# Performance work log

Hardware: AMD Instinct MI355X
Metric: run time of the kernel (lower is better)

## Reference

```python
import jax, jax.numpy as jnp
import numpy as np

# FP4 E2M1 representable magnitudes (sign handled separately)
_FP4_GRID = np.array([0.0, 0.5, 1.0, 1.5, 2.0, 3.0, 4.0, 6.0], dtype=np.float32)
_FP4_MIDS = (_FP4_GRID[:-1] + _FP4_GRID[1:]) / 2.0  # round-to-nearest boundaries


def fp4_quant_dequant(w):
    """Per-tensor absmax-scaled round-to-nearest FP4 (E2M1) fake quantization."""
    grid = jnp.asarray(_FP4_GRID, dtype=w.dtype)
    mids = jnp.asarray(_FP4_MIDS, dtype=w.dtype)
    scale = jnp.max(jnp.abs(w)) / 6.0  # map absmax -> top FP4 level
    a = jnp.abs(w) / scale
    idx = jnp.searchsorted(mids, a)  # nearest grid index via boundary search
    return grid[idx] * jnp.sign(w) * scale


def fp4_linear(x, W, b):
    # dequantized-weight matmul + bias, as in FP4Linear
    Wq = fp4_quant_dequant(W)
    return x @ Wq.T + b


def setup_inputs() -> dict:
    key = jax.random.key(0)
    k1, k2, k3, k4, k5 = jax.random.split(key, 5)
    B, D_IN, D_H, D_OUT = 8192, 2048, 8192, 2048
    x = jax.random.normal(k1, (B, D_IN), dtype=jnp.float32)
    W1 = jax.random.normal(k2, (D_H, D_IN), dtype=jnp.float32) * 0.02
    b1 = jax.random.normal(k3, (D_H,), dtype=jnp.float32) * 0.02
    W2 = jax.random.normal(k4, (D_OUT, D_H), dtype=jnp.float32) * 0.02
    b2 = jax.random.normal(k5, (D_OUT,), dtype=jnp.float32) * 0.02
    return {"x": x, "W1": W1, "b1": b1, "W2": W2, "b2": b2}


def reference(x, W1, b1, W2, b2):
    h = jax.nn.relu(fp4_linear(x, W1, b1))  # [B, hidden]
    y = fp4_linear(h, W2, b2)                # [B, out]
    return y
```

## Files before the change

kernel.cpp:

```cpp
#include <hip/hip_runtime.h>
#include <hip/hip_bf16.h>
#include <stdint.h>

typedef __attribute__((ext_vector_type(8))) short short8;
typedef __attribute__((ext_vector_type(4))) float f32x4;

#define AS1 __attribute__((address_space(1)))
#define AS3 __attribute__((address_space(3)))

static __device__ __forceinline__ unsigned short f2bf(float f) {
    unsigned int u = __float_as_uint(f);
    u += 0x7FFFu + ((u >> 16) & 1u);
    return (unsigned short)(u >> 16);
}

__global__ void init_amax(unsigned int* amax) {
    if (threadIdx.x < 2) amax[threadIdx.x] = 0u;
}

__global__ void absmax_kernel(const float4* __restrict__ w, size_t n4,
                              unsigned int* __restrict__ out) {
    float m = 0.0f;
    size_t i = (size_t)blockIdx.x * blockDim.x + threadIdx.x;
    size_t stride = (size_t)gridDim.x * blockDim.x;
    for (; i < n4; i += stride) {
        float4 v = w[i];
        m = fmaxf(m, fmaxf(fmaxf(fabsf(v.x), fabsf(v.y)),
                           fmaxf(fabsf(v.z), fabsf(v.w))));
    }
    #pragma unroll
    for (int off = 32; off > 0; off >>= 1)
        m = fmaxf(m, __shfl_down(m, off, 64));
    __shared__ float sm[4];
    int lane = threadIdx.x & 63, wid = threadIdx.x >> 6;
    if (lane == 0) sm[wid] = m;
    __syncthreads();
    if (threadIdx.x == 0) {
        float bm = fmaxf(fmaxf(sm[0], sm[1]), fmaxf(sm[2], sm[3]));
        atomicMax(out, __float_as_uint(bm));
    }
}

static __device__ __forceinline__ unsigned short quant_one(float wv, float scale) {
    float a = fabsf(wv) / scale;
    int idx = (a > 0.25f) + (a > 0.75f) + (a > 1.25f) + (a > 1.75f)
            + (a > 2.5f)  + (a > 3.5f)  + (a > 5.0f);
    const unsigned long long lo = 0x3FC03F803F000000ull;
    const unsigned long long hi = 0x40C0408040404000ull;
    unsigned long long tab = (idx < 4) ? lo : hi;
    unsigned short mag = (unsigned short)(tab >> ((idx & 3) * 16));
    unsigned short sgn = (unsigned short)((__float_as_uint(wv) >> 16) & 0x8000u);
    return (unsigned short)(mag | sgn);
}

__global__ void quant_kernel(const float4* __restrict__ w, size_t n4,
                             const unsigned int* __restrict__ amax,
                             ushort4* __restrict__ q) {
    const float scale = __uint_as_float(*amax) / 6.0f;
    size_t i = (size_t)blockIdx.x * blockDim.x + threadIdx.x;
    size_t stride = (size_t)gridDim.x * blockDim.x;
    for (; i < n4; i += stride) {
        float4 v = w[i];
        ushort4 o;
        o.x = quant_one(v.x, scale);
        o.y = quant_one(v.y, scale);
        o.z = quant_one(v.z, scale);
        o.w = quant_one(v.w, scale);
        q[i] = o;
    }
}

__global__ void cast_bf16_kernel(const float4* __restrict__ x, size_t n4,
                                 ushort4* __restrict__ o) {
    size_t i = (size_t)blockIdx.x * blockDim.x + threadIdx.x;
    size_t stride = (size_t)gridDim.x * blockDim.x;
    for (; i < n4; i += stride) {
        float4 v = x[i];
        ushort4 r;
        r.x = f2bf(v.x); r.y = f2bf(v.y); r.z = f2bf(v.z); r.w = f2bf(v.w);
        o[i] = r;
    }
}


#define GLL(gp, dst)                                                    \
    __builtin_amdgcn_global_load_lds((const AS1 unsigned int*)(gp),     \
        (AS3 unsigned int*)(dst), 16, 0, 0)

#define STG(gp, ldsoff)                                       \
    do {                                                      \
        GLL((gp) + goff0, lds + (ldsoff) + tid * 16);         \
        GLL((gp) + goff1, lds + (ldsoff) + 8192 + tid * 16);  \
    } while (0)

#define LD4(dst, base, s0)                                                    \
    do {                                                                      \
        _Pragma("unroll") for (int _i = 0; _i < 4; ++_i)                      \
            dst[_i] = *(const short8*)((base) + ((s0) + _i * 2) * 1024);      \
    } while (0)

#define MFG(AH, ARR, BRR)                                                      \
    do {                                                                       \
        _Pragma("unroll") for (int _i = 0; _i < 4; ++_i)                       \
            _Pragma("unroll") for (int _j = 0; _j < 4; ++_j)                   \
                acc[(AH) * 4 + _i][_j] =                                       \
                    __builtin_amdgcn_mfma_f32_16x16x32_bf16(                   \
                        ARR[_i], BRR[_j], acc[(AH) * 4 + _i][_j], 0, 0, 0);    \
    } while (0)

#define BAR()  __builtin_amdgcn_s_barrier()
#define PRIO(x) __builtin_amdgcn_s_setprio(x)
#define SCHB() __builtin_amdgcn_sched_barrier(0)
#define LGKM(n) do { SCHB(); asm volatile("s_waitcnt lgkmcnt(" #n ")"); SCHB(); } while (0)

#define KTILE(ldsB_, ldsA_, MA1, kA1, oA1, MORE, kNXT, oB0, oB1, oA0, VMODE)   \
    do {                                                                       \
        LD4(bE, ldsB_, 0);                                  \
        LD4(aP, ldsA_, 0);                                     \
        LD4(aQ, ldsA_, 8);                                     \
        if (MA1) STG(pA1 + (kA1), oA1);                                        \
        LGKM(4);                                \
        PRIO(1); MFG(0, aP, bE); PRIO(0);                                      \
        LD4(bO, ldsB_, 1);                                        \
        LD4(aP, ldsA_, 1);                                     \
        LGKM(8);                               \
        PRIO(1); MFG(1, aQ, bE); PRIO(0);                                      \
        LD4(aQ, ldsA_, 9);                                     \
        LGKM(4);                              \
        PRIO(1); MFG(0, aP, bO); PRIO(0);                                      \
        LGKM(0);                            \
        BAR();                                                                 \
        if (MORE) { STG(pB0 + (kNXT), oB0); STG(pB1 + (kNXT), oB1);            \
                    STG(pA0 + (kNXT), oA0); }                                  \
        SCHB();                                                                \
        PRIO(1); MFG(1, aQ, bO); PRIO(0);                                      \
        if (VMODE == 2) { asm volatile("s_waitcnt vmcnt(6)"); }                \
        if (VMODE == 1) { asm volatile("s_waitcnt vmcnt(0)"); }                \
        BAR();                                                                 \
    } while (0)

template <int RELU_BF16>
__global__ __launch_bounds__(512, 2)
void gemm8(const unsigned short* __restrict__ A,
           const unsigned short* __restrict__ B,
           const float* __restrict__ bias,
           const unsigned int* __restrict__ amax,
           float* __restrict__ outF,
           unsigned short* __restrict__ outH,
           int M, int N, int K, int gx) {
    __shared__ __align__(16) char lds[131072];

    const int tid  = threadIdx.x;
    const int lane = tid & 63;
    const int wid  = tid >> 6;
    const int wm   = wid >> 2;
    const int wn   = wid & 3;

    const int nwg = gridDim.x;
    const int wg  = blockIdx.x;
    const int swz = (wg & 7) * (nwg >> 3) + (wg >> 3);
    const int bx  = swz % gx;
    const int by  = swz / gx;
    const int col0 = bx * 256;
    const int row0 = by * 256;

    int sp = ((lane & 15) << 6) + ((lane >> 4) << 4);
    sp ^= ((sp >> 9) & 1) << 5;

    const char* ldsA_E = lds + wm * 16384 + sp;
    const char* ldsB_E = lds + 32768 + (wn >> 1) * 16384 + (wn & 1) * 8192 + sp;
    const char* ldsA_O = ldsA_E + 65536;
    const char* ldsB_O = ldsB_E + 65536;

    int goff0, goff1;
    {
        int o = tid * 16;
        int s = o >> 10, b = o & 1023;
        b ^= ((b >> 9) & 1) << 5;
        goff0 = (((s >> 1) << 4) + (b >> 6)) * K + ((s & 1) << 5) + ((b & 63) >> 1);
        o = 8192 + tid * 16;
        s = o >> 10; b = o & 1023;
        b ^= ((b >> 9) & 1) << 5;
        goff1 = (((s >> 1) << 4) + (b >> 6)) * K + ((s & 1) << 5) + ((b & 63) >> 1);
    }
    const unsigned short* pA0 = A + (size_t)row0 * K;
    const unsigned short* pA1 = A + (size_t)(row0 + 128) * K;
    const unsigned short* pB0 = B + (size_t)col0 * K;
    const unsigned short* pB1 = B + (size_t)(col0 + 128) * K;

    STG(pB0, 32768); STG(pB1, 49152); STG(pA0, 0); STG(pA1, 16384);
    STG(pB0 + 64, 98304); STG(pB1 + 64, 114688); STG(pA0 + 64, 65536);
    asm volatile("s_waitcnt vmcnt(6)");
    BAR();

    f32x4 acc[8][4] = {};
    short8 aP[4], aQ[4], bE[4], bO[4];
    const int NIT = K >> 7;

    for (int it = 0; it < NIT - 1; ++it) {
        const int o0 = it * 128;
        KTILE(ldsB_E, ldsA_E, 1, o0 + 64, 81920,
              1, o0 + 128, 32768, 49152, 0, 2);
        KTILE(ldsB_O, ldsA_O, 1, o0 + 128, 16384,
              1, o0 + 192, 98304, 114688, 65536, 2);
    }
    {
        const int o0 = (NIT - 1) * 128;
        KTILE(ldsB_E, ldsA_E, 1, o0 + 64, 81920,
              0, 0, 0, 0, 0, 1);
        KTILE(ldsB_O, ldsA_O, 0, 0, 0,
              0, 0, 0, 0, 0, 0);
    }

    const float scale = __uint_as_float(*amax) / 6.0f;
    #pragma unroll
    for (int j = 0; j < 4; ++j) {
        const int col = col0 + wn * 64 + j * 16 + (lane & 15);
        const float bvv = bias[col];
        #pragma unroll
        for (int i = 0; i < 8; ++i) {
            const int rbase = row0 + wm * 128 + i * 16 + (lane >> 4) * 4;
            #pragma unroll
            for (int r = 0; r < 4; ++r) {
                float v = acc[i][j][r] * scale + bvv;
                if (RELU_BF16) {
                    v = fmaxf(v, 0.0f);
                    outH[(size_t)(rbase + r) * N + col] = f2bf(v);
                } else {
                    outF[(size_t)(rbase + r) * N + col] = v;
                }
            }
        }
    }
}

extern "C" void kernel_launch(void* const* d_in, const int* in_sizes, int n_in,
                              void* d_out, int out_size, void* d_ws, size_t ws_size,
                              hipStream_t stream) {
    const float* x  = (const float*)d_in[0];
    const float* W1 = (const float*)d_in[1];
    const float* b1 = (const float*)d_in[2];
    const float* W2 = (const float*)d_in[3];
    const float* b2 = (const float*)d_in[4];
    float* out = (float*)d_out;

    const int Bm = 8192, Din = 2048, Dh = 8192, Dout = 2048;
    const size_t nW1 = (size_t)Dh * Din;
    const size_t nW2 = (size_t)Dout * Dh;
    const size_t nX  = (size_t)Bm * Din;
    const size_t nH  = (size_t)Bm * Dh;

    const size_t need = 256 + 2 * (nW1 + nW2 + nX + nH);
    if (ws_size < need) return;

    uint8_t* ws = (uint8_t*)d_ws;
    unsigned int*   amax = (unsigned int*)ws;
    unsigned short* Q1 = (unsigned short*)(ws + 256);
    unsigned short* Q2 = Q1 + nW1;
    unsigned short* Xb = Q2 + nW2;
    unsigned short* H  = Xb + nX;

    init_amax<<<1, 64, 0, stream>>>(amax);
    absmax_kernel<<<1024, 256, 0, stream>>>((const float4*)W1, nW1 / 4, amax + 0);
    absmax_kernel<<<1024, 256, 0, stream>>>((const float4*)W2, nW2 / 4, amax + 1);
    quant_kernel<<<2048, 256, 0, stream>>>((const float4*)W1, nW1 / 4, amax + 0, (ushort4*)Q1);
    quant_kernel<<<2048, 256, 0, stream>>>((const float4*)W2, nW2 / 4, amax + 1, (ushort4*)Q2);
    cast_bf16_kernel<<<2048, 256, 0, stream>>>((const float4*)x, nX / 4, (ushort4*)Xb);

    gemm8<1><<<dim3((Dh / 256) * (Bm / 256)), 512, 0, stream>>>(
        Xb, Q1, b1, amax + 0, nullptr, H, Bm, Dh, Din, Dh / 256);
    gemm8<0><<<dim3((Dout / 256) * (Bm / 256)), 512, 0, stream>>>(
        H, Q2, b2, amax + 1, out, nullptr, Bm, Dout, Dh, Dout / 256);
}
```

Measured before the change: 569.1 us.

## Switch GEMM to 32x32x16 bf16 MFMA with restructured LDS fragment loads

Replaces the 16x16x32 MFMA tiling with 32x32x16 bf16 MFMAs. Each wave now holds a 4x2 grid of 32x32 accumulators, and the LDS read addressing is recomputed to build 32x32 fragments. The prefetch schedule moves both A halves together and the vmcnt waits change to match. The larger MFMA shape cuts the number of LDS fragment loads and MFMA issues per FLOP, at the cost of a new LDS access pattern that may introduce bank conflicts and a different pipelining order.

After: 1.308 ms, median of 2. +129.9%, slower.

```diff
diff --git a/kernel.cpp b/kernel.cpp
--- a/kernel.cpp
+++ b/kernel.cpp
@@ -3,7 +3,7 @@
 #include <stdint.h>
 
 typedef __attribute__((ext_vector_type(8))) short short8;
-typedef __attribute__((ext_vector_type(4))) float f32x4;
+typedef __attribute__((ext_vector_type(16))) float f32x16;
 
 #define AS1 __attribute__((address_space(1)))
 #define AS3 __attribute__((address_space(3)))
@@ -93,19 +93,30 @@
         GLL((gp) + goff1, lds + (ldsoff) + 8192 + tid * 16);  \
     } while (0)
 
-#define LD4(dst, base, s0)                                                    \
+#define LDA8(dst, base, ksbase)                                               \
     do {                                                                      \
-        _Pragma("unroll") for (int _i = 0; _i < 4; ++_i)                      \
-            dst[_i] = *(const short8*)((base) + ((s0) + _i * 2) * 1024);      \
-    } while (0)
-
-#define MFG(AH, ARR, BRR)                                                      \
+        _Pragma("unroll") for (int _m = 0; _m < 4; ++_m)                      \
+            _Pragma("unroll") for (int _k = 0; _k < 2; ++_k)                  \
+                dst[_m * 2 + _k] = *(const short8*)((base) + _m * 4096 +      \
+                                                    sp32[(ksbase) + _k]);     \
+    } while (0)
+
+#define LDB4(dst, base, ksbase)                                               \
+    do {                                                                      \
+        _Pragma("unroll") for (int _n = 0; _n < 2; ++_n)                      \
+            _Pragma("unroll") for (int _k = 0; _k < 2; ++_k)                  \
+                dst[_n * 2 + _k] = *(const short8*)((base) + _n * 4096 +      \
+                                                    sp32[(ksbase) + _k]);     \
+    } while (0)
+
+#define MFK(ARR, BRR)                                                          \
     do {                                                                       \
-        _Pragma("unroll") for (int _i = 0; _i < 4; ++_i)                       \
-            _Pragma("unroll") for (int _j = 0; _j < 4; ++_j)                   \
-                acc[(AH) * 4 + _i][_j] =                                       \
-                    __builtin_amdgcn_mfma_f32_16x16x32_bf16(                   \
-                        ARR[_i], BRR[_j], acc[(AH) * 4 + _i][_j], 0, 0, 0);    \
+        _Pragma("unroll") for (int _m = 0; _m < 4; ++_m)                       \
+            _Pragma("unroll") for (int _n = 0; _n < 2; ++_n)                   \
+                _Pragma("unroll") for (int _k = 0; _k < 2; ++_k)               \
+                    acc[_m][_n] = __builtin_amdgcn_mfma_f32_32x32x16_bf16(     \
+                        ARR[_m * 2 + _k], BRR[_n * 2 + _k], acc[_m][_n],       \
+                        0, 0, 0);                                              \
     } while (0)
 
 #define BAR()  __builtin_amdgcn_s_barrier()
@@ -113,28 +124,21 @@
 #define SCHB() __builtin_amdgcn_sched_barrier(0)
 #define LGKM(n) do { SCHB(); asm volatile("s_waitcnt lgkmcnt(" #n ")"); SCHB(); } while (0)
 
-#define KTILE(ldsB_, ldsA_, MA1, kA1, oA1, MORE, kNXT, oB0, oB1, oA0, VMODE)   \
+#define KTILE32(ldsB_, ldsA_, MA, kA, oA0_, oA1_, MB, kB, oB0_, oB1_, VMODE)   \
     do {                                                                       \
-        LD4(bE, ldsB_, 0);                                  \
-        LD4(aP, ldsA_, 0);                                     \
-        LD4(aQ, ldsA_, 8);                                     \
-        if (MA1) STG(pA1 + (kA1), oA1);                                        \
-        LGKM(4);                                \
-        PRIO(1); MFG(0, aP, bE); PRIO(0);                                      \
-        LD4(bO, ldsB_, 1);                                        \
-        LD4(aP, ldsA_, 1);                                     \
-        LGKM(8);                               \
-        PRIO(1); MFG(1, aQ, bE); PRIO(0);                                      \
-        LD4(aQ, ldsA_, 9);                                     \
-        LGKM(4);                              \
-        PRIO(1); MFG(0, aP, bO); PRIO(0);                                      \
+        LDA8(aP, ldsA_, 0);                       \
+        LDB4(b0, ldsB_, 0);                             \
+        if (MA) { STG(pA0 + (kA), oA0_); STG(pA1 + (kA), oA1_); }              \
+        LDB4(b1, ldsB_, 2);                                    \
+        LDA8(aQ, ldsA_, 2);                                    \
+        LGKM(12);                            \
+        PRIO(1); MFK(aP, b0); PRIO(0);                                         \
         LGKM(0);                            \
         BAR();                                                                 \
-        if (MORE) { STG(pB0 + (kNXT), oB0); STG(pB1 + (kNXT), oB1);            \
-                    STG(pA0 + (kNXT), oA0); }                                  \
+        if (MB) { STG(pB0 + (kB), oB0_); STG(pB1 + (kB), oB1_); }              \
         SCHB();                                                                \
-        PRIO(1); MFG(1, aQ, bO); PRIO(0);                                      \
-        if (VMODE == 2) { asm volatile("s_waitcnt vmcnt(6)"); }                \
+        PRIO(1); MFK(aQ, b1); PRIO(0);                                         \
+        if (VMODE == 2) { asm volatile("s_waitcnt vmcnt(4)"); }                \
         if (VMODE == 1) { asm volatile("s_waitcnt vmcnt(0)"); }                \
         BAR();                                                                 \
     } while (0)
@@ -164,11 +168,20 @@
     const int col0 = bx * 256;
     const int row0 = by * 256;
 
-    int sp = ((lane & 15) << 6) + ((lane >> 4) << 4);
-    sp ^= ((sp >> 9) & 1) << 5;
-
-    const char* ldsA_E = lds + wm * 16384 + sp;
-    const char* ldsB_E = lds + 32768 + (wn >> 1) * 16384 + (wn & 1) * 8192 + sp;
+    int sp32[4];
+    {
+        const int l = lane;
+        const int base16 = ((l >> 4) & 1) * 2048;
+        const int inner0 = ((l & 15) << 6) + (((l >> 5) & 1) << 4);
+        const int flip = ((l >> 3) & 1) << 5;
+        #pragma unroll
+        for (int ks = 0; ks < 4; ++ks)
+            sp32[ks] = base16 + (ks >> 1) * 1024 +
+                       ((inner0 + ((ks & 1) << 5)) ^ flip);
+    }
+
+    const char* ldsA_E = lds + wm * 16384;
+    const char* ldsB_E = lds + 32768 + wn * 8192;
     const char* ldsA_O = ldsA_E + 65536;
     const char* ldsB_O = ldsB_E + 65536;
 
@@ -189,45 +202,46 @@
     const unsigned short* pB1 = B + (size_t)(col0 + 128) * K;
 
     STG(pB0, 32768); STG(pB1, 49152); STG(pA0, 0); STG(pA1, 16384);
-    STG(pB0 + 64, 98304); STG(pB1 + 64, 114688); STG(pA0 + 64, 65536);
-    asm volatile("s_waitcnt vmcnt(6)");
+    STG(pB0 + 64, 98304); STG(pB1 + 64, 114688);
+    asm volatile("s_waitcnt vmcnt(4)");
     BAR();
 
-    f32x4 acc[8][4] = {};
-    short8 aP[4], aQ[4], bE[4], bO[4];
-    const int NIT = K >> 7;
-
-    for (int it = 0; it < NIT - 1; ++it) {
+    f32x16 acc[4][2] = {};
+    short8 aP[8], aQ[8], b0[4], b1[4];
+    const int NIT2 = K >> 7;
+
+    for (int it = 0; it < NIT2 - 1; ++it) {
         const int o0 = it * 128;
-        KTILE(ldsB_E, ldsA_E, 1, o0 + 64, 81920,
-              1, o0 + 128, 32768, 49152, 0, 2);
-        KTILE(ldsB_O, ldsA_O, 1, o0 + 128, 16384,
-              1, o0 + 192, 98304, 114688, 65536, 2);
+        KTILE32(ldsB_E, ldsA_E, 1, o0 + 64, 65536, 81920,
+                1, o0 + 128, 32768, 49152, 2);
+        KTILE32(ldsB_O, ldsA_O, 1, o0 + 128, 0, 16384,
+                1, o0 + 192, 98304, 114688, 2);
     }
     {
-        const int o0 = (NIT - 1) * 128;
-        KTILE(ldsB_E, ldsA_E, 1, o0 + 64, 81920,
-              0, 0, 0, 0, 0, 1);
-        KTILE(ldsB_O, ldsA_O, 0, 0, 0,
-              0, 0, 0, 0, 0, 0);
+        const int o0 = (NIT2 - 1) * 128;
+        KTILE32(ldsB_E, ldsA_E, 1, o0 + 64, 65536, 81920,
+                0, 0, 0, 0, 1);
+        KTILE32(ldsB_O, ldsA_O, 0, 0, 0, 0,
+                0, 0, 0, 0, 0);
     }
 
     const float scale = __uint_as_float(*amax) / 6.0f;
     #pragma unroll
-    for (int j = 0; j < 4; ++j) {
-        const int col = col0 + wn * 64 + j * 16 + (lane & 15);
+    for (int nb = 0; nb < 2; ++nb) {
+        const int col = col0 + wn * 64 + nb * 32 + (lane & 31);
         const float bvv = bias[col];
         #pragma unroll
-        for (int i = 0; i < 8; ++i) {
-            const int rbase = row0 + wm * 128 + i * 16 + (lane >> 4) * 4;
+        for (int mb = 0; mb < 4; ++mb) {
+            const int rbase = row0 + wm * 128 + mb * 32 + ((lane >> 5) & 1) * 4;
             #pragma unroll
-            for (int r = 0; r < 4; ++r) {
-                float v = acc[i][j][r] * scale + bvv;
+            for (int r = 0; r < 16; ++r) {
+                const int row = rbase + (r & 3) + 8 * (r >> 2);
+                float v = acc[mb][nb][r] * scale + bvv;
                 if (RELU_BF16) {
                     v = fmaxf(v, 0.0f);
-                    outH[(size_t)(rbase + r) * N + col] = f2bf(v);
+                    outH[(size_t)row * N + col] = f2bf(v);
                 } else {
-                    outF[(size_t)(rbase + r) * N + col] = v;
+                    outF[(size_t)row * N + col] = v;
                 }
             }
         }
```

## Store hidden activations in tiled layout, stage fp32 epilogue via LDS, regroup tiles

Applied to the files above, without the earlier changes.

The first GEMM now writes H in a 16x16-tiled layout, so the second GEMM's A-operand loads read contiguous 512-byte chunks instead of strided rows. The fp32 output epilogue of the second GEMM is staged through LDS with a swizzle, so each thread writes 16-byte vectors to global memory instead of scattered 4-byte stores. Workgroup-to-tile mapping changes to per-XCD rectangular chunks of width cw, intended to improve L2 reuse. The cost is a more complex addressing scheme and extra barriers in the epilogue.

Result: faster. 534.2 us (median of 3 runs) (-6.1%).

```diff
diff --git a/kernel.cpp b/kernel.cpp
--- a/kernel.cpp
+++ b/kernel.cpp
@@ -87,11 +87,20 @@
     __builtin_amdgcn_global_load_lds((const AS1 unsigned int*)(gp),     \
         (AS3 unsigned int*)(dst), 16, 0, 0)
 
-#define STG(gp, ldsoff)                                       \
-    do {                                                      \
-        GLL((gp) + goff0, lds + (ldsoff) + tid * 16);         \
-        GLL((gp) + goff1, lds + (ldsoff) + 8192 + tid * 16);  \
-    } while (0)
+#define STGA(gp, ldsoff)                                        \
+    do {                                                        \
+        GLL((gp) + goffA0, lds + (ldsoff) + tid * 16);          \
+        GLL((gp) + goffA1, lds + (ldsoff) + 8192 + tid * 16);   \
+    } while (0)
+
+#define STGB(gp, ldsoff)                                        \
+    do {                                                        \
+        GLL((gp) + goffB0, lds + (ldsoff) + tid * 16);          \
+        GLL((gp) + goffB1, lds + (ldsoff) + 8192 + tid * 16);   \
+    } while (0)
+
+#define KAB(e) ((size_t)(e) * (LAYA ? 32 : 2))
+#define KBB(e) ((size_t)(e) * 2)
 
 #define LD4(dst, base, s0)                                                    \
     do {                                                                      \
@@ -118,7 +127,7 @@
         LD4(bE, ldsB_, 0);                                  \
         LD4(aP, ldsA_, 0);                                     \
         LD4(aQ, ldsA_, 8);                                     \
-        if (MA1) STG(pA1 + (kA1), oA1);                                        \
+        if (MA1) STGA(pA1 + KAB(kA1), oA1);                                    \
         LGKM(4);                                \
         PRIO(1); MFG(0, aP, bE); PRIO(0);                                      \
         LD4(bO, ldsB_, 1);                                        \
@@ -130,8 +139,8 @@
         PRIO(1); MFG(0, aP, bO); PRIO(0);                                      \
         LGKM(0);                            \
         BAR();                                                                 \
-        if (MORE) { STG(pB0 + (kNXT), oB0); STG(pB1 + (kNXT), oB1);            \
-                    STG(pA0 + (kNXT), oA0); }                                  \
+        if (MORE) { STGB(pB0 + KBB(kNXT), oB0); STGB(pB1 + KBB(kNXT), oB1);    \
+                    STGA(pA0 + KAB(kNXT), oA0); }                              \
         SCHB();                                                                \
         PRIO(1); MFG(1, aQ, bO); PRIO(0);                                      \
         if (VMODE == 2) { asm volatile("s_waitcnt vmcnt(6)"); }                \
@@ -139,15 +148,15 @@
         BAR();                                                                 \
     } while (0)
 
-template <int RELU_BF16>
+template <int RELU_BF16, int LAYA>
 __global__ __launch_bounds__(512, 2)
-void gemm8(const unsigned short* __restrict__ A,
+void gemm8(const char* __restrict__ A,
            const unsigned short* __restrict__ B,
            const float* __restrict__ bias,
            const unsigned int* __restrict__ amax,
            float* __restrict__ outF,
-           unsigned short* __restrict__ outH,
-           int M, int N, int K, int gx) {
+           char* __restrict__ outH,
+           int M, int N, int K, int gx, int cw) {
     __shared__ __align__(16) char lds[131072];
 
     const int tid  = threadIdx.x;
@@ -158,9 +167,14 @@
 
     const int nwg = gridDim.x;
     const int wg  = blockIdx.x;
-    const int swz = (wg & 7) * (nwg >> 3) + (wg >> 3);
-    const int bx  = swz % gx;
-    const int by  = swz / gx;
+    const int c   = wg & 7;
+    const int idx = wg >> 3;
+    const int nc  = nwg >> 3;
+    const int cxc = gx / cw;
+    const int ox  = (c % cxc) * cw;
+    const int oy  = (c / cxc) * (nc / cw);
+    const int bx  = ox + idx % cw;
+    const int by  = oy + idx / cw;
     const int col0 = bx * 256;
     const int row0 = by * 256;
 
@@ -172,24 +186,32 @@
     const char* ldsA_O = ldsA_E + 65536;
     const char* ldsB_O = ldsB_E + 65536;
 
-    int goff0, goff1;
+    int goffA0, goffA1, goffB0, goffB1;
     {
-        int o = tid * 16;
-        int s = o >> 10, b = o & 1023;
-        b ^= ((b >> 9) & 1) << 5;
-        goff0 = (((s >> 1) << 4) + (b >> 6)) * K + ((s & 1) << 5) + ((b & 63) >> 1);
-        o = 8192 + tid * 16;
-        s = o >> 10; b = o & 1023;
-        b ^= ((b >> 9) & 1) << 5;
-        goff1 = (((s >> 1) << 4) + (b >> 6)) * K + ((s & 1) << 5) + ((b & 63) >> 1);
-    }
-    const unsigned short* pA0 = A + (size_t)row0 * K;
-    const unsigned short* pA1 = A + (size_t)(row0 + 128) * K;
-    const unsigned short* pB0 = B + (size_t)col0 * K;
-    const unsigned short* pB1 = B + (size_t)(col0 + 128) * K;
-
-    STG(pB0, 32768); STG(pB1, 49152); STG(pA0, 0); STG(pA1, 16384);
-    STG(pB0 + 64, 98304); STG(pB1 + 64, 114688); STG(pA0 + 64, 65536);
+        #pragma unroll
+        for (int h = 0; h < 2; ++h) {
+            int o = h * 8192 + tid * 16;
+            int s = o >> 10, b = o & 1023;
+            b ^= ((b >> 9) & 1) << 5;
+            int row = ((s >> 1) << 4) + (b >> 6);
+            int k   = ((s & 1) << 5) + ((b & 63) >> 1);
+            int gB  = (row * K + k) * 2;
+            int gA  = LAYA ? ((row >> 4) * 262144 + (k >> 4) * 512 +
+                              (row & 3) * 128 + ((row >> 2) & 3) * 32 + (k & 15) * 2)
+                           : gB;
+            if (h == 0) { goffA0 = gA; goffB0 = gB; }
+            else        { goffA1 = gA; goffB1 = gB; }
+        }
+    }
+    const char* pA0 = A + (LAYA ? (size_t)row0 * 16384 : (size_t)row0 * K * 2);
+    const char* pA1 = A + (LAYA ? (size_t)(row0 + 128) * 16384
+                                : (size_t)(row0 + 128) * K * 2);
+    const char* pB0 = (const char*)B + (size_t)col0 * K * 2;
+    const char* pB1 = (const char*)B + (size_t)(col0 + 128) * K * 2;
+
+    STGB(pB0, 32768); STGB(pB1, 49152); STGA(pA0, 0); STGA(pA1, 16384);
+    STGB(pB0 + KBB(64), 98304); STGB(pB1 + KBB(64), 114688);
+    STGA(pA0 + KAB(64), 65536);
     asm volatile("s_waitcnt vmcnt(6)");
     BAR();
 
@@ -213,23 +235,57 @@
     }
 
     const float scale = __uint_as_float(*amax) / 6.0f;
-    #pragma unroll
-    for (int j = 0; j < 4; ++j) {
-        const int col = col0 + wn * 64 + j * 16 + (lane & 15);
-        const float bvv = bias[col];
+
+    if (RELU_BF16) {
+        const int gbit = (lane >> 4) * 32 + (lane & 15) * 2;
         #pragma unroll
-        for (int i = 0; i < 8; ++i) {
-            const int rbase = row0 + wm * 128 + i * 16 + (lane >> 4) * 4;
+        for (int j = 0; j < 4; ++j) {
+            const int col = col0 + wn * 64 + j * 16 + (lane & 15);
+            const float bvv = bias[col];
+            const size_t ktb = (size_t)((col0 >> 4) + wn * 4 + j) * 512;
             #pragma unroll
-            for (int r = 0; r < 4; ++r) {
-                float v = acc[i][j][r] * scale + bvv;
-                if (RELU_BF16) {
-                    v = fmaxf(v, 0.0f);
-                    outH[(size_t)(rbase + r) * N + col] = f2bf(v);
-                } else {
-                    outF[(size_t)(rbase + r) * N + col] = v;
+            for (int i = 0; i < 8; ++i) {
+                const size_t rtb = (size_t)(((row0 + wm * 128) >> 4) + i) * 262144;
+                #pragma unroll
+                for (int r = 0; r < 4; ++r) {
+                    float v = fmaxf(acc[i][j][r] * scale + bvv, 0.0f);
+                    *(unsigned short*)(outH + rtb + ktb + r * 128 + gbit) = f2bf(v);
                 }
             }
+        }
+    } else {
+        #pragma unroll
+        for (int p = 0; p < 2; ++p) {
+            if (wm == p) {
+                #pragma unroll
+                for (int j = 0; j < 4; ++j) {
+                    const int colb = wn * 64 + j * 16 + (lane & 15);
+                    const float bvv = bias[col0 + colb];
+                    #pragma unroll
+                    for (int i = 0; i < 8; ++i) {
+                        #pragma unroll
+                        for (int r = 0; r < 4; ++r) {
+                            const int row_l = i * 16 + (lane >> 4) * 4 + r;
+                            const int blk = (colb >> 2) ^ (((row_l >> 2) & 3) << 2);
+                            *(float*)(lds + row_l * 1024 + blk * 16 + (colb & 3) * 4)
+                                = acc[i][j][r] * scale + bvv;
+                        }
+                    }
+                }
+            }
+            asm volatile("s_waitcnt lgkmcnt(0)");
+            BAR();
+            #pragma unroll
+            for (int q = 0; q < 16; ++q) {
+                const int flat  = q * 8192 + tid * 16;
+                const int row_l = flat >> 10;
+                const int blk0  = (flat >> 4) & 63;
+                const int blk   = blk0 ^ (((row_l >> 2) & 3) << 2);
+                f32x4 v = *(const f32x4*)(lds + row_l * 1024 + blk * 16);
+                *(f32x4*)(outF + (size_t)(row0 + p * 128 + row_l) * N
+                                 + col0 + blk0 * 4) = v;
+            }
+            BAR();
         }
     }
 }
@@ -258,7 +314,7 @@
     unsigned short* Q1 = (unsigned short*)(ws + 256);
     unsigned short* Q2 = Q1 + nW1;
     unsigned short* Xb = Q2 + nW2;
-    unsigned short* H  = Xb + nX;
+    char*           H  = (char*)(Xb + nX);
 
     init_amax<<<1, 64, 0, stream>>>(amax);
     absmax_kernel<<<1024, 256, 0, stream>>>((const float4*)W1, nW1 / 4, amax + 0);
@@ -267,8 +323,10 @@
     quant_kernel<<<2048, 256, 0, stream>>>((const float4*)W2, nW2 / 4, amax + 1, (ushort4*)Q2);
     cast_bf16_kernel<<<2048, 256, 0, stream>>>((const float4*)x, nX / 4, (ushort4*)Xb);
 
-    gemm8<1><<<dim3((Dh / 256) * (Bm / 256)), 512, 0, stream>>>(
-        Xb, Q1, b1, amax + 0, nullptr, H, Bm, Dh, Din, Dh / 256);
-    gemm8<0><<<dim3((Dout / 256) * (Bm / 256)), 512, 0, stream>>>(
-        H, Q2, b2, amax + 1, out, nullptr, Bm, Dout, Dh, Dout / 256);
-}
+    gemm8<1, 0><<<dim3((Dh / 256) * (Bm / 256)), 512, 0, stream>>>(
+        (const char*)Xb, Q1, b1, amax + 0, nullptr, H,
+        Bm, Dh, Din, Dh / 256, 16);
+    gemm8<0, 1><<<dim3((Dout / 256) * (Bm / 256)), 512, 0, stream>>>(
+        H, Q2, b2, amax + 1, out, nullptr,
+        Bm, Dout, Dh, Dout / 256, 8);
+}
```
